# Kernel optimization log

Measured on AMD Instinct MI355X. Metric: run time of the kernel, lower is better.

The kernel has to match this reference:

```python
import jax, jax.numpy as jnp
import numpy as np

B, S, E, H = 32, 256, 768, 32
D = E // H  # head_dim = 24


def setup_inputs() -> dict:
    key = jax.random.key(0)
    ks = jax.random.split(key, 10)
    w_sc = 1.0 / np.sqrt(E)  # xavier-ish init scale for weights
    return {
        "feats": jax.random.normal(ks[0], (B, S, E), jnp.float32),
        "attn_bias": jax.random.normal(ks[1], (B, H, S, S), jnp.float32),
        "delta_pos": jax.random.normal(ks[2], (B, S, S, 3), jnp.float32),
        "Wq": jax.random.normal(ks[3], (E, E), jnp.float32) * w_sc,
        "bq": jnp.zeros((E,), jnp.float32),
        "Wk": jax.random.normal(ks[4], (E, E), jnp.float32) * w_sc,
        "bk": jnp.zeros((E,), jnp.float32),
        "Wv": jax.random.normal(ks[5], (E, E), jnp.float32) * w_sc,
        "bv": jnp.zeros((E,), jnp.float32),
        "Wfx": jax.random.normal(ks[6], (E,), jnp.float32) * w_sc,
        "Wfy": jax.random.normal(ks[7], (E,), jnp.float32) * w_sc,
        "Wfz": jax.random.normal(ks[8], (E,), jnp.float32) * w_sc,
    }


def reference(feats, attn_bias, delta_pos, Wq, bq, Wk, bk, Wv, bv, Wfx, Wfy, Wfz):
    b, s, e = feats.shape
    h = attn_bias.shape[1]
    d = e // h
    scaling = d ** -0.5
    # q/k/v projections; q scaled by 1/sqrt(head_dim)
    q = ((feats @ Wq + bq) * scaling).reshape(b, s, h, d).transpose(0, 2, 1, 3)  # (b,h,s,d)
    k = (feats @ Wk + bk).reshape(b, s, h, d).transpose(0, 2, 1, 3)              # (b,h,t,d)
    v = (feats @ Wv + bv).reshape(b, s, h, d).transpose(0, 2, 1, 3)              # (b,h,t,d)
    scores = jnp.einsum('bhsd,bhtd->bhst', q, k) + attn_bias
    probs = jax.nn.softmax(scores, axis=-1)  # dropout p in eval -> identity
    # rot_attn_probs = probs[...,None] * delta_pos[:,None] fused into one contraction:
    # (b,h,s,t) * (b,s,t,3) contracted with (b,h,t,c) over t -> (b,s,3,h,c)
    attn = jnp.einsum('bhst,bstx,bhtc->bsxhc', probs, delta_pos, v)
    attn = attn.reshape(b, s, 3, e)  # flatten (h,c) -> e
    out_x = attn[..., 0, :] @ Wfx  # (b,s)
    out_y = attn[..., 1, :] @ Wfy
    out_z = attn[..., 2, :] @ Wfz
    return jnp.stack([out_x, out_y, out_z], axis=-1)  # (b,s,3)
```

## Files before the change

kernel.cpp:

```cpp
#include <hip/hip_runtime.h>
#include <hip/hip_bf16.h>

#define B_ 32
#define S_ 256
#define E_ 768
#define H_ 32
#define D_ 24
#define NTOT 1664

typedef __hip_bfloat16 bf16;
typedef __attribute__((ext_vector_type(8))) short short8;
typedef __attribute__((ext_vector_type(4))) float floatx4;
typedef __attribute__((ext_vector_type(2))) float f32x2;

#define GLOAD_LDS16(g, l)                                          \
  __builtin_amdgcn_global_load_lds(                                \
      (const __attribute__((address_space(1))) void*)(g),          \
      (__attribute__((address_space(3))) void*)(l), 16, 0, 0)

#define CAST_BLKS 6144
#define QK_BLKS   288
#define VW_BLKS   391

__global__ __launch_bounds__(256) void prep_fused(
    const float* __restrict__ feats, bf16* __restrict__ fb,
    const float* __restrict__ Wq, const float* __restrict__ Wk,
    const float* __restrict__ Wv,
    const float* __restrict__ bq, const float* __restrict__ bk,
    const float* __restrict__ bv,
    const float* __restrict__ Wfx, const float* __restrict__ Wfy,
    const float* __restrict__ Wfz,
    bf16* __restrict__ Wt, float* __restrict__ biasf)
{
  __shared__ float tile[64][65];
  const float qscale = 0.20412414523193154f;
  int bid = blockIdx.x;

  if (bid < CAST_BLKS) {
    int i = bid * 256 + threadIdx.x;
    float4 v = reinterpret_cast<const float4*>(feats)[i];
    union { ushort4 u; bf16 b[4]; } pk;
    pk.b[0] = (bf16)v.x; pk.b[1] = (bf16)v.y;
    pk.b[2] = (bf16)v.z; pk.b[3] = (bf16)v.w;
    reinterpret_cast<ushort4*>(fb)[i] = pk.u;
    return;
  }
  if (bid < CAST_BLKS + QK_BLKS) {
    int id = bid - CAST_BLKS;
    int n0 = (id % 24) * 64;
    int k0 = (id / 24) * 64;
    int j = threadIdx.x & 63, i4 = threadIdx.x >> 6;
    bool isq = (n0 < 768);
    const float* W = isq ? Wq : Wk;
    int nc = isq ? n0 : n0 - 768;
    float sc = isq ? qscale : 1.0f;
    #pragma unroll
    for (int r = 0; r < 16; r++) {
      int i = r * 4 + i4;
      tile[i][j] = W[(size_t)(k0 + i) * E_ + nc + j] * sc;
    }
    __syncthreads();
    #pragma unroll
    for (int r = 0; r < 16; r++) {
      int jj = r * 4 + i4;
      Wt[(size_t)(n0 + jj) * E_ + k0 + j] = (bf16)tile[j][jj];
    }
    return;
  }
  int gid = (bid - CAST_BLKS - QK_BLKS) * 256 + threadIdx.x;
  if (gid < 128 * E_) {
    int n = 1536 + gid / E_, k = gid % E_;
    float val = 0.f;
    if (n < 1632) {
      int nn = n - 1536, x = nn >> 5, h = nn & 31;
      const float* Wf = (x == 0) ? Wfx : (x == 1 ? Wfy : Wfz);
      #pragma unroll
      for (int c = 0; c < D_; c++)
        val += Wv[(size_t)k * E_ + h * D_ + c] * Wf[h * D_ + c];
    }
    Wt[(size_t)n * E_ + k] = (bf16)val;
  } else {
    int n = gid - 128 * E_;
    if (n < NTOT) {
      float val;
      if (n < 768) {
        val = bq[n] * qscale;
      } else if (n < 1536) {
        val = bk[n - 768];
      } else if (n < 1632) {
        int nn = n - 1536, x = nn >> 5, h = nn & 31;
        const float* Wf = (x == 0) ? Wfx : (x == 1 ? Wfy : Wfz);
        float s = 0.f;
        #pragma unroll
        for (int c = 0; c < D_; c++)
          s += bv[h * D_ + c] * Wf[h * D_ + c];
        val = s;
      } else {
        val = 0.f;
      }
      biasf[n] = val;
    }
  }
}

__global__ __launch_bounds__(256) void gemm_qkv(
    const bf16* __restrict__ A, const bf16* __restrict__ Wt,
    const float* __restrict__ biasf,
    bf16* __restrict__ qout, bf16* __restrict__ kout,
    float* __restrict__ vwout)
{
  __shared__ __align__(16) short As[128 * 64];
  __shared__ __align__(16) short Bs[128 * 64];
  int tid = threadIdx.x;
  int m0 = blockIdx.y * 128, n0 = blockIdx.x * 128;
  int wave = tid >> 6, lane = tid & 63;
  int wm = (wave >> 1) * 64, wn = (wave & 1) * 64;
  int fr = lane & 15, quad = lane >> 4;

  int srow = tid >> 3;
  int schunk = (tid & 7) ^ (srow & 7);
  const bf16* Asrc = A + (size_t)(m0 + srow) * E_ + schunk * 8;
  const bf16* Bsrc = Wt + (size_t)(n0 + srow) * E_ + schunk * 8;
  short* AsW = As + wave * 512;
  short* BsW = Bs + wave * 512;

  floatx4 acc[4][4];
  const floatx4 zero = {0.f, 0.f, 0.f, 0.f};
  #pragma unroll
  for (int i = 0; i < 4; i++)
    #pragma unroll
    for (int j = 0; j < 4; j++) acc[i][j] = zero;

  int ra[4][2], rb[4][2];
  #pragma unroll
  for (int t = 0; t < 4; t++) {
    int rowa = wm + t * 16 + fr;
    int rowb = wn + t * 16 + fr;
    #pragma unroll
    for (int kk = 0; kk < 2; kk++) {
      ra[t][kk] = rowa * 64 + (((quad + kk * 4) ^ (rowa & 7)) * 8);
      rb[t][kk] = rowb * 64 + (((quad + kk * 4) ^ (rowb & 7)) * 8);
    }
  }

  for (int k0 = 0; k0 < E_; k0 += 64) {
    if (k0) __syncthreads();
    #pragma unroll
    for (int j = 0; j < 4; j++) {
      GLOAD_LDS16(Asrc + (size_t)(j * 32) * E_ + k0, AsW + j * 2048);
      GLOAD_LDS16(Bsrc + (size_t)(j * 32) * E_ + k0, BsW + j * 2048);
    }
    __syncthreads();
    #pragma unroll
    for (int kk = 0; kk < 2; kk++) {
      short8 af[4], bfr[4];
      #pragma unroll
      for (int t = 0; t < 4; t++)
        af[t] = *reinterpret_cast<const short8*>(&As[ra[t][kk]]);
      #pragma unroll
      for (int t = 0; t < 4; t++)
        bfr[t] = *reinterpret_cast<const short8*>(&Bs[rb[t][kk]]);
      #pragma unroll
      for (int ti = 0; ti < 4; ti++)
        #pragma unroll
        for (int tj = 0; tj < 4; tj++)
          acc[ti][tj] = __builtin_amdgcn_mfma_f32_16x16x32_bf16(
              af[ti], bfr[tj], acc[ti][tj], 0, 0, 0);
    }
  }

  #pragma unroll
  for (int ti = 0; ti < 4; ti++) {
    #pragma unroll
    for (int tj = 0; tj < 4; tj++) {
      int n = n0 + wn + tj * 16 + fr;
      float bias = biasf[n];
      #pragma unroll
      for (int r = 0; r < 4; r++) {
        int m = m0 + wm + ti * 16 + quad * 4 + r;
        int b = m >> 8, s = m & 255;
        float val = acc[ti][tj][r] + bias;
        if (n < 768) {
          int h = n / 24, d = n - h * 24;
          qout[(((size_t)b * H_ + h) * S_ + s) * D_ + d] = (bf16)val;
        } else if (n < 1536) {
          int n2 = n - 768;
          int h = n2 / 24, d = n2 - h * 24;
          kout[(((size_t)b * H_ + h) * S_ + s) * D_ + d] = (bf16)val;
        } else if (n < 1632) {
          int nn = n - 1536, x = nn >> 5, hh = nn & 31;
          vwout[(((size_t)x * B_ + b) * H_ + hh) * S_ + s] = val;
        }
      }
    }
  }
}

__global__ __launch_bounds__(256) void attn_kernel(
    const bf16* __restrict__ qg, const bf16* __restrict__ kg,
    const float* __restrict__ vwg, const float* __restrict__ biasg,
    const float* __restrict__ dpg, float* __restrict__ part)
{
  __shared__ __align__(16) float ql[64 * 26];
  int blk = blockIdx.x;
  int b = blk & 31;
  int u = blk >> 5;
  int h = u & 31;
  int st = (u >> 5) * 64;
  int bh = b * H_ + h;
  int tid = threadIdx.x, wave = tid >> 6, lane = tid & 63;
  int t0 = lane * 4;

  f32x2 kr[4][12];
  {
    const short8* kp = reinterpret_cast<const short8*>(
        kg + ((size_t)bh * S_ + t0) * D_);
    #pragma unroll
    for (int v = 0; v < 12; v++) {
      short8 kk = kp[v];
      int row = v / 3, seg = v % 3;
      #pragma unroll
      for (int p2 = 0; p2 < 4; p2++) {
        union { short u; bf16 bb; } a, c;
        a.u = kk[2 * p2]; c.u = kk[2 * p2 + 1];
        f32x2 t2; t2.x = (float)a.bb; t2.y = (float)c.bb;
        kr[row][seg * 4 + p2] = t2;
      }
    }
  }
  float vwr[3][4];
  #pragma unroll
  for (int x = 0; x < 3; x++) {
    float4 v4 = *reinterpret_cast<const float4*>(
        vwg + (((size_t)x * B_ + b) * H_ + h) * S_ + t0);
    vwr[x][0] = v4.x; vwr[x][1] = v4.y; vwr[x][2] = v4.z; vwr[x][3] = v4.w;
  }
  {
    int r = tid >> 2, c0 = (tid & 3) * 6;
    const bf16* qrow = qg + ((size_t)bh * S_ + st + r) * D_ + c0;
    #pragma unroll
    for (int i = 0; i < 6; i++) ql[r * 26 + c0 + i] = (float)qrow[i];
  }
  __syncthreads();

  const float* biasbh = biasg + (size_t)bh * S_ * S_;
  const float* dpb    = dpg + (size_t)b * S_ * S_ * 3;

  float4 nb, nd0, nd1, nd2;
  {
    int s0 = st + wave;
    nb = *reinterpret_cast<const float4*>(biasbh + (size_t)s0 * S_ + t0);
    const float* dpr = dpb + (size_t)s0 * S_ * 3 + (size_t)t0 * 3;
    nd0 = *reinterpret_cast<const float4*>(dpr);
    nd1 = *reinterpret_cast<const float4*>(dpr + 4);
    nd2 = *reinterpret_cast<const float4*>(dpr + 8);
  }

  for (int si = 0; si < 16; si++) {
    float4 bias4 = nb, e0 = nd0, e1 = nd1, e2 = nd2;
    int nsi = (si + 1 < 16) ? si + 1 : 0;
    int ns = st + nsi * 4 + wave;
    nb = *reinterpret_cast<const float4*>(biasbh + (size_t)ns * S_ + t0);
    const float* dpn = dpb + (size_t)ns * S_ * 3 + (size_t)t0 * 3;
    nd0 = *reinterpret_cast<const float4*>(dpn);
    nd1 = *reinterpret_cast<const float4*>(dpn + 4);
    nd2 = *reinterpret_cast<const float4*>(dpn + 8);

    int sr = si * 4 + wave;
    int s  = st + sr;

    f32x2 sc2[4];
    #pragma unroll
    for (int j = 0; j < 4; j++) { sc2[j].x = 0.f; sc2[j].y = 0.f; }
    #pragma unroll
    for (int i = 0; i < 12; i++) {
      f32x2 qd = *reinterpret_cast<const f32x2*>(&ql[sr * 26 + 2 * i]);
      #pragma unroll
      for (int j = 0; j < 4; j++) sc2[j] += qd * kr[j][i];
    }
    float p[4];
    p[0] = __expf(sc2[0].x + sc2[0].y + bias4.x - 4.0f);
    p[1] = __expf(sc2[1].x + sc2[1].y + bias4.y - 4.0f);
    p[2] = __expf(sc2[2].x + sc2[2].y + bias4.z - 4.0f);
    p[3] = __expf(sc2[3].x + sc2[3].y + bias4.w - 4.0f);
    float l = (p[0] + p[1]) + (p[2] + p[3]);

    float dx[4] = {e0.x, e0.w, e1.z, e2.y};
    float dy[4] = {e0.y, e1.x, e1.w, e2.z};
    float dz[4] = {e0.z, e1.y, e2.x, e2.w};

    float ax = 0.f, ay = 0.f, az = 0.f;
    #pragma unroll
    for (int j = 0; j < 4; j++) {
      ax = fmaf(p[j] * dx[j], vwr[0][j], ax);
      ay = fmaf(p[j] * dy[j], vwr[1][j], ay);
      az = fmaf(p[j] * dz[j], vwr[2][j], az);
    }
    #pragma unroll
    for (int o = 32; o; o >>= 1) {
      ax += __shfl_xor(ax, o);
      ay += __shfl_xor(ay, o);
      az += __shfl_xor(az, o);
      l  += __shfl_xor(l, o);
    }
    if (lane == 0) {
      float inv = 1.0f / l;
      float* op = part + ((size_t)bh * S_ + s) * 3;
      op[0] = ax * inv; op[1] = ay * inv; op[2] = az * inv;
    }
  }
}

__global__ __launch_bounds__(256) void reduce_h(
    const float* __restrict__ part, float* __restrict__ out)
{
  int k = blockIdx.x * 256 + threadIdx.x;
  int b = k / (S_ * 3);
  int r = k - b * (S_ * 3);
  const float* p = part + (size_t)b * H_ * S_ * 3 + r;
  float acc = 0.f;
  #pragma unroll
  for (int h = 0; h < H_; h++) acc += p[(size_t)h * S_ * 3];
  out[k] = acc;
}

extern "C" void kernel_launch(void* const* d_in, const int* in_sizes, int n_in,
                              void* d_out, int out_size, void* d_ws, size_t ws_size,
                              hipStream_t stream)
{
  const float* feats     = (const float*)d_in[0];
  const float* attn_bias = (const float*)d_in[1];
  const float* delta_pos = (const float*)d_in[2];
  const float* Wq        = (const float*)d_in[3];
  const float* bq        = (const float*)d_in[4];
  const float* Wk        = (const float*)d_in[5];
  const float* bk        = (const float*)d_in[6];
  const float* Wv        = (const float*)d_in[7];
  const float* bv        = (const float*)d_in[8];
  const float* Wfx       = (const float*)d_in[9];
  const float* Wfy       = (const float*)d_in[10];
  const float* Wfz       = (const float*)d_in[11];

  char* ws = (char*)d_ws;
  size_t off = 0;
  auto alloc = [&](size_t bytes) -> void* {
    void* p = ws + off;
    off = (off + bytes + 255) & ~(size_t)255;
    return p;
  };
  bf16*  ws_fb   = (bf16*) alloc((size_t)B_ * S_ * E_ * 2);
  bf16*  ws_q    = (bf16*) alloc((size_t)B_ * H_ * S_ * D_ * 2);
  bf16*  ws_k    = (bf16*) alloc((size_t)B_ * H_ * S_ * D_ * 2);
  float* ws_vw   = (float*)alloc((size_t)3 * B_ * H_ * S_ * 4);
  bf16*  ws_Wt   = (bf16*) alloc((size_t)NTOT * E_ * 2);
  float* ws_bias = (float*)alloc((size_t)NTOT * 4);
  float* ws_part = (float*)alloc((size_t)B_ * H_ * S_ * 3 * 4);

  prep_fused<<<CAST_BLKS + QK_BLKS + VW_BLKS, 256, 0, stream>>>(
      feats, ws_fb, Wq, Wk, Wv, bq, bk, bv, Wfx, Wfy, Wfz, ws_Wt, ws_bias);

  gemm_qkv<<<dim3(NTOT / 128, B_ * S_ / 128), 256, 0, stream>>>(
      ws_fb, ws_Wt, ws_bias, ws_q, ws_k, ws_vw);

  attn_kernel<<<B_ * H_ * 4, 256, 0, stream>>>(ws_q, ws_k, ws_vw, attn_bias,
                                               delta_pos, ws_part);

  reduce_h<<<(B_ * S_ * 3) / 256, 256, 0, stream>>>(ws_part, (float*)d_out);
}
```

Before: 531.3 us.

## Split attention key dimension in two halves, defer softmax normalization to reduce

The attention kernel now splits the 256 keys into two halves handled by separate blocks, doubling the grid and halving per-thread registers (kr, vwr, loads). Each half writes unnormalized x/y/z sums plus its partial denominator as a float4, and the head-reduction kernel combines both halves and divides. This targets higher occupancy (launch bounds raised to 8) and more parallelism for the memory-bound bias/delta_pos stream. In exchange, loads become 8-byte instead of 16-byte, the partial buffer grows, and the reduce kernel does more work.

```diff
diff --git a/kernel.cpp b/kernel.cpp
--- a/kernel.cpp
+++ b/kernel.cpp
@@ -196,7 +196,7 @@
   }
 }
 
-__global__ __launch_bounds__(256) void attn_kernel(
+__global__ __launch_bounds__(256, 8) void attn_kernel(
     const bf16* __restrict__ qg, const bf16* __restrict__ kg,
     const float* __restrict__ vwg, const float* __restrict__ biasg,
     const float* __restrict__ dpg, float* __restrict__ part)
@@ -206,17 +206,19 @@
   int b = blk & 31;
   int u = blk >> 5;
   int h = u & 31;
-  int st = (u >> 5) * 64;
+  int v2 = u >> 5;
+  int st = (v2 & 3) * 64;
+  int th = v2 >> 2;
   int bh = b * H_ + h;
   int tid = threadIdx.x, wave = tid >> 6, lane = tid & 63;
-  int t0 = lane * 4;
-
-  f32x2 kr[4][12];
+  int t0 = th * 128 + lane * 2;
+
+  f32x2 kr[2][12];
   {
     const short8* kp = reinterpret_cast<const short8*>(
         kg + ((size_t)bh * S_ + t0) * D_);
     #pragma unroll
-    for (int v = 0; v < 12; v++) {
+    for (int v = 0; v < 6; v++) {
       short8 kk = kp[v];
       int row = v / 3, seg = v % 3;
       #pragma unroll
@@ -228,12 +230,12 @@
       }
     }
   }
-  float vwr[3][4];
+  float vwr[3][2];
   #pragma unroll
   for (int x = 0; x < 3; x++) {
-    float4 v4 = *reinterpret_cast<const float4*>(
+    f32x2 vv = *reinterpret_cast<const f32x2*>(
         vwg + (((size_t)x * B_ + b) * H_ + h) * S_ + t0);
-    vwr[x][0] = v4.x; vwr[x][1] = v4.y; vwr[x][2] = v4.z; vwr[x][3] = v4.w;
+    vwr[x][0] = vv.x; vwr[x][1] = vv.y;
   }
   {
     int r = tid >> 2, c0 = (tid & 3) * 6;
@@ -243,59 +245,48 @@
   }
   __syncthreads();
 
-  const float* biasbh = biasg + (size_t)bh * S_ * S_;
+  const float* biasbh = biasg + (size_t)bh * S_ * S_ + th * 128;
   const float* dpb    = dpg + (size_t)b * S_ * S_ * 3;
 
-  float4 nb, nd0, nd1, nd2;
+  f32x2 nb, nd0, nd1, nd2;
   {
     int s0 = st + wave;
-    nb = *reinterpret_cast<const float4*>(biasbh + (size_t)s0 * S_ + t0);
+    nb = *reinterpret_cast<const f32x2*>(biasbh + (size_t)s0 * S_ + lane * 2);
     const float* dpr = dpb + (size_t)s0 * S_ * 3 + (size_t)t0 * 3;
-    nd0 = *reinterpret_cast<const float4*>(dpr);
-    nd1 = *reinterpret_cast<const float4*>(dpr + 4);
-    nd2 = *reinterpret_cast<const float4*>(dpr + 8);
+    nd0 = *reinterpret_cast<const f32x2*>(dpr);
+    nd1 = *reinterpret_cast<const f32x2*>(dpr + 2);
+    nd2 = *reinterpret_cast<const f32x2*>(dpr + 4);
   }
 
   for (int si = 0; si < 16; si++) {
-    float4 bias4 = nb, e0 = nd0, e1 = nd1, e2 = nd2;
+    f32x2 bias2 = nb, e0 = nd0, e1 = nd1, e2 = nd2;
     int nsi = (si + 1 < 16) ? si + 1 : 0;
     int ns = st + nsi * 4 + wave;
-    nb = *reinterpret_cast<const float4*>(biasbh + (size_t)ns * S_ + t0);
+    nb = *reinterpret_cast<const f32x2*>(biasbh + (size_t)ns * S_ + lane * 2);
     const float* dpn = dpb + (size_t)ns * S_ * 3 + (size_t)t0 * 3;
-    nd0 = *reinterpret_cast<const float4*>(dpn);
-    nd1 = *reinterpret_cast<const float4*>(dpn + 4);
-    nd2 = *reinterpret_cast<const float4*>(dpn + 8);
+    nd0 = *reinterpret_cast<const f32x2*>(dpn);
+    nd1 = *reinterpret_cast<const f32x2*>(dpn + 2);
+    nd2 = *reinterpret_cast<const f32x2*>(dpn + 4);
 
     int sr = si * 4 + wave;
     int s  = st + sr;
 
-    f32x2 sc2[4];
-    #pragma unroll
-    for (int j = 0; j < 4; j++) { sc2[j].x = 0.f; sc2[j].y = 0.f; }
+    f32x2 sc0, sc1;
+    sc0.x = 0.f; sc0.y = 0.f; sc1.x = 0.f; sc1.y = 0.f;
     #pragma unroll
     for (int i = 0; i < 12; i++) {
       f32x2 qd = *reinterpret_cast<const f32x2*>(&ql[sr * 26 + 2 * i]);
-      #pragma unroll
-      for (int j = 0; j < 4; j++) sc2[j] += qd * kr[j][i];
-    }
-    float p[4];
-    p[0] = __expf(sc2[0].x + sc2[0].y + bias4.x - 4.0f);
-    p[1] = __expf(sc2[1].x + sc2[1].y + bias4.y - 4.0f);
-    p[2] = __expf(sc2[2].x + sc2[2].y + bias4.z - 4.0f);
-    p[3] = __expf(sc2[3].x + sc2[3].y + bias4.w - 4.0f);
-    float l = (p[0] + p[1]) + (p[2] + p[3]);
-
-    float dx[4] = {e0.x, e0.w, e1.z, e2.y};
-    float dy[4] = {e0.y, e1.x, e1.w, e2.z};
-    float dz[4] = {e0.z, e1.y, e2.x, e2.w};
-
-    float ax = 0.f, ay = 0.f, az = 0.f;
-    #pragma unroll
-    for (int j = 0; j < 4; j++) {
-      ax = fmaf(p[j] * dx[j], vwr[0][j], ax);
-      ay = fmaf(p[j] * dy[j], vwr[1][j], ay);
-      az = fmaf(p[j] * dz[j], vwr[2][j], az);
-    }
+      sc0 += qd * kr[0][i];
+      sc1 += qd * kr[1][i];
+    }
+    float p0 = __expf(sc0.x + sc0.y + bias2.x - 4.0f);
+    float p1 = __expf(sc1.x + sc1.y + bias2.y - 4.0f);
+    float l = p0 + p1;
+
+    float ax = fmaf(p0 * e0.x, vwr[0][0], p1 * e1.y * vwr[0][1]);
+    float ay = fmaf(p0 * e0.y, vwr[1][0], p1 * e2.x * vwr[1][1]);
+    float az = fmaf(p0 * e1.x, vwr[2][0], p1 * e2.y * vwr[2][1]);
+
     #pragma unroll
     for (int o = 32; o; o >>= 1) {
       ax += __shfl_xor(ax, o);
@@ -304,9 +295,9 @@
       l  += __shfl_xor(l, o);
     }
     if (lane == 0) {
-      float inv = 1.0f / l;
-      float* op = part + ((size_t)bh * S_ + s) * 3;
-      op[0] = ax * inv; op[1] = ay * inv; op[2] = az * inv;
+      float4 o4; o4.x = ax; o4.y = ay; o4.z = az; o4.w = l;
+      *reinterpret_cast<float4*>(
+          part + (((size_t)bh * S_ + s) * 2 + th) * 4) = o4;
     }
   }
 }
@@ -317,10 +308,15 @@
   int k = blockIdx.x * 256 + threadIdx.x;
   int b = k / (S_ * 3);
   int r = k - b * (S_ * 3);
-  const float* p = part + (size_t)b * H_ * S_ * 3 + r;
+  int s = r / 3, x = r - s * 3;
   float acc = 0.f;
   #pragma unroll
-  for (int h = 0; h < H_; h++) acc += p[(size_t)h * S_ * 3];
+  for (int h = 0; h < H_; h++) {
+    const float* p = part + (((size_t)(b * H_ + h) * S_ + s) * 2) * 4;
+    float A = p[x] + p[4 + x];
+    float l = p[3] + p[7];
+    acc += A / l;
+  }
   out[k] = acc;
 }
 
@@ -354,7 +350,7 @@
   float* ws_vw   = (float*)alloc((size_t)3 * B_ * H_ * S_ * 4);
   bf16*  ws_Wt   = (bf16*) alloc((size_t)NTOT * E_ * 2);
   float* ws_bias = (float*)alloc((size_t)NTOT * 4);
-  float* ws_part = (float*)alloc((size_t)B_ * H_ * S_ * 3 * 4);
+  float* ws_part = (float*)alloc((size_t)B_ * H_ * S_ * 2 * 4 * 4);
 
   prep_fused<<<CAST_BLKS + QK_BLKS + VW_BLKS, 256, 0, stream>>>(
       feats, ws_fb, Wq, Wk, Wv, bq, bk, bv, Wfx, Wfy, Wfz, ws_Wt, ws_bias);
@@ -362,7 +358,7 @@
   gemm_qkv<<<dim3(NTOT / 128, B_ * S_ / 128), 256, 0, stream>>>(
       ws_fb, ws_Wt, ws_bias, ws_q, ws_k, ws_vw);
 
-  attn_kernel<<<B_ * H_ * 4, 256, 0, stream>>>(ws_q, ws_k, ws_vw, attn_bias,
+  attn_kernel<<<B_ * H_ * 8, 256, 0, stream>>>(ws_q, ws_k, ws_vw, attn_bias,
                                                delta_pos, ws_part);
 
   reduce_h<<<(B_ * S_ * 3) / 256, 256, 0, stream>>>(ws_part, (float*)d_out);
```

New measurement: 912.9 us. 1.72x slower.
